# Kernel optimization log

Measured on AMD Instinct MI355X. Metric: run time of the kernel, lower is better.

Reference implementation:

```python
import jax, jax.numpy as jnp
import numpy as np

B, S, H, FF, E, K, A = 2, 2048, 2048, 8192, 8, 2, 64
P = 3 * H * FF                      # num_ffn_params (gate + up + down)
NS = int(P * 1e-4)                  # num_sparse = 5033
TEMP = 1.0                          # mask_temperature


def setup_inputs() -> dict:
    key = jax.random.key(0)
    ks = jax.random.split(key, 9)
    f32 = jnp.float32
    return {
        "hidden_states": jax.random.normal(ks[0], (B, S, H), f32),
        "gate_w": jax.random.normal(ks[1], (FF, H), f32) * 0.02,
        "up_w": jax.random.normal(ks[2], (FF, H), f32) * 0.02,
        "down_w": jax.random.normal(ks[3], (H, FF), f32) * 0.02,
        "router_w": jax.random.normal(ks[4], (E, H), f32) * 0.01,
        "mask_logits": jax.random.normal(ks[5], (P,), f32) * 0.01,
        "atoms": jax.random.normal(ks[6], (A, NS), f32) * 0.02,
        "expert_atom_weights": jax.random.normal(ks[7], (E, A), f32) * 0.1,
        "importance": jax.random.normal(ks[8], (E, NS), f32) * 0.1,
    }


def reference(hidden_states, gate_w, up_w, down_w, router_w, mask_logits,
              atoms, expert_atom_weights, importance):
    b, s, h = hidden_states.shape
    x = hidden_states.reshape(-1, h)                      # (T, H) tokens

    # ---- SRDERouter: gate -> clamp -> top-k -> softmax over top-k ----
    router_logits = jnp.clip(x @ router_w.T, -50.0, 50.0)  # (T, E)
    top_w, top_idx = jax.lax.top_k(router_logits, K)       # (T, K)
    router_weights = jax.nn.softmax(top_w, axis=-1)        # (T, K)

    # ---- LearnedMaskSelector (eval path: no gumbel noise), straight-through ----
    noisy = jnp.clip(mask_logits / TEMP, -50.0, 50.0)      # (P,)
    soft_mask = jax.nn.sigmoid(noisy)
    _, mask_idx = jax.lax.top_k(noisy, NS)                 # (NS,) positions in param space
    hard_mask = jnp.zeros_like(soft_mask).at[mask_idx].set(1.0)
    mask = hard_mask - jax.lax.stop_gradient(soft_mask) + soft_mask  # (P,)

    # ---- SharedDeltaVocabulary + SparseExpert importance weighting ----
    atom_w = jax.nn.softmax(expert_atom_weights, axis=-1)  # (E, A)
    deltas = atom_w @ atoms                                # (E, NS)
    weighted_deltas = deltas * jax.nn.sigmoid(importance)  # (E, NS)

    # ---- per-token gather of top-k expert deltas, weighted combine ----
    tok_deltas = weighted_deltas[top_idx]                  # (T, K, NS) irregular gather
    combined = jnp.einsum('tk,tks->ts', router_weights, tok_deltas)  # (T, NS)
    mean_delta = combined.mean(axis=0)                     # (NS,) batch-averaged delta

    # ---- scatter sparse delta into flat FFN param space, apply mask ----
    flat = jnp.concatenate([gate_w.ravel(), up_w.ravel(), down_w.ravel()])  # (P,)
    delta_full = jnp.zeros_like(flat).at[mask_idx].set(mean_delta) * mask
    new_flat = flat + delta_full
    n1 = FF * H
    gw = new_flat[:n1].reshape(FF, H)
    uw = new_flat[n1:2 * n1].reshape(FF, H)
    dw = new_flat[2 * n1:].reshape(H, FF)

    # ---- SwiGLU FFN with delta-perturbed params ----
    hidden = jax.nn.silu(x @ gw.T) * (x @ uw.T)            # (T, FF)
    out = (hidden @ dw.T).reshape(b, s, h)

    # ---- load-balancing aux loss ----
    probs = jax.nn.softmax(router_logits, axis=-1)         # (T, E)
    frac = jax.nn.one_hot(top_idx, E, dtype=probs.dtype).sum(1).mean(0) / K  # (E,)
    aux_loss = E * jnp.sum(probs.mean(0) * frac)

    return out, router_logits, router_weights, top_idx, aux_loss
```

## Files before the change

kernel.cpp:

```cpp
#include <hip/hip_runtime.h>
#include <stdint.h>

#define DEV __device__ __forceinline__

typedef __attribute__((ext_vector_type(8))) short short8;
typedef __attribute__((ext_vector_type(4))) float f32x4;

constexpr int       Td  = 4096;
constexpr int       Hd  = 2048;
constexpr int       FFd = 8192;
constexpr int       NSd = 5033;
constexpr long long n1  = 16777216LL;
constexpr long long Pn  = 50331648LL;
constexpr int NBINS    = 16384;
constexpr int CAND_CAP = 8192;
constexpr unsigned KEY_MIN = 0xBC75C28Fu;

constexpr size_t OUT_LOGITS = 8388608;
constexpr size_t OUT_RW     = 8421376;
constexpr size_t OUT_TI     = 8429568;
constexpr size_t OUT_AUX    = 8437760;

constexpr size_t OFF_W    = 0;
constexpr size_t OFF_X    = 100663296;
constexpr size_t OFF_HID  = 117440512;
constexpr size_t OFF_HIST = 184549376;
constexpr size_t OFF_META = OFF_HIST + NBINS * 4;
constexpr size_t OFF_CAND = OFF_META + 256;
constexpr size_t OFF_MIDX = OFF_CAND + CAND_CAP * 8;
constexpr size_t OFF_MD   = OFF_MIDX + 20480;

DEV unsigned short f2bf(float f) {
    unsigned u = __float_as_uint(f);
    u += 0x7FFFu + ((u >> 16) & 1u);
    return (unsigned short)(u >> 16);
}
DEV unsigned keyof(float v) {
    v = fminf(50.f, fmaxf(-50.f, v));
    unsigned b = __float_as_uint(v);
    return (b & 0x80000000u) ? ~b : (b | 0x80000000u);
}

#define GL16(gsrc, ldst) __builtin_amdgcn_global_load_lds( \
    (const __attribute__((address_space(1))) unsigned int*)(const void*)(gsrc), \
    (__attribute__((address_space(3))) unsigned int*)(void*)(ldst), 16, 0, 0)

#define SWZC(r, c) ((c) ^ (((r) & 7) << 3))
#define SWZ(r, c)  (((r) * 64) + SWZC(r, c))

__global__ __launch_bounds__(256) void k_cvt_x(const float4* __restrict__ x,
                                               ushort4* __restrict__ o, int n4) {
    int stride = gridDim.x * blockDim.x;
    for (int i = blockIdx.x * blockDim.x + threadIdx.x; i < n4; i += stride) {
        float4 v = x[i];
        ushort4 r; r.x = f2bf(v.x); r.y = f2bf(v.y); r.z = f2bf(v.z); r.w = f2bf(v.w);
        o[i] = r;
    }
}

__global__ __launch_bounds__(256) void k_cvt_w(const float4* __restrict__ g,
                                               const float4* __restrict__ u,
                                               const float4* __restrict__ d,
                                               ushort4* __restrict__ o) {
    const long long n1_4 = n1 / 4, n4 = Pn / 4;
    long long stride = (long long)gridDim.x * blockDim.x;
    for (long long i = blockIdx.x * (long long)blockDim.x + threadIdx.x; i < n4; i += stride) {
        float4 v = (i < n1_4) ? g[i] : (i < 2 * n1_4) ? u[i - n1_4] : d[i - 2 * n1_4];
        ushort4 r; r.x = f2bf(v.x); r.y = f2bf(v.y); r.z = f2bf(v.z); r.w = f2bf(v.w);
        o[i] = r;
    }
}

__global__ __launch_bounds__(1024) void k_router(const float* __restrict__ x,
                                                 const float* __restrict__ rw,
                                                 float* __restrict__ out,
                                                 float* __restrict__ meta_f) {
    __shared__ float sacc[24];
    int tid = threadIdx.x;
    if (tid < 24) sacc[tid] = 0.f;
    __syncthreads();
    int wid = tid >> 6, lane = tid & 63;
    int t = blockIdx.x * 16 + wid;
    const float4* xr = (const float4*)(x + (size_t)t * Hd);
    double acc[8] = {0, 0, 0, 0, 0, 0, 0, 0};
    for (int i = 0; i < 8; ++i) {
        float4 xv = xr[i * 64 + lane];
#pragma unroll
        for (int e = 0; e < 8; ++e) {
            float4 wv = ((const float4*)(rw + (size_t)e * Hd))[i * 64 + lane];
            acc[e] += (double)xv.x * wv.x + (double)xv.y * wv.y +
                      (double)xv.z * wv.z + (double)xv.w * wv.w;
        }
    }
#pragma unroll
    for (int e = 0; e < 8; ++e)
        for (int s = 32; s; s >>= 1) acc[e] += __shfl_xor(acc[e], s, 64);
    if (lane == 0) {
        float lg[8];
#pragma unroll
        for (int e = 0; e < 8; ++e) lg[e] = fminf(50.f, fmaxf(-50.f, (float)acc[e]));
        float* lo = out + OUT_LOGITS + (size_t)t * 8;
#pragma unroll
        for (int e = 0; e < 8; ++e) lo[e] = lg[e];
        int i1 = 0;
        for (int e = 1; e < 8; ++e) if (lg[e] > lg[i1]) i1 = e;
        int i2 = (i1 == 0) ? 1 : 0;
        for (int e = 0; e < 8; ++e) if (e != i1 && lg[e] > lg[i2]) i2 = e;
        float e2 = expf(lg[i2] - lg[i1]);
        float r1 = 1.f / (1.f + e2), r2 = e2 / (1.f + e2);
        out[OUT_RW + (size_t)t * 2]     = r1;
        out[OUT_RW + (size_t)t * 2 + 1] = r2;
        out[OUT_TI + (size_t)t * 2]     = (float)i1;
        out[OUT_TI + (size_t)t * 2 + 1] = (float)i2;
        float m = lg[0];
        for (int e = 1; e < 8; ++e) m = fmaxf(m, lg[e]);
        float p[8], s = 0.f;
#pragma unroll
        for (int e = 0; e < 8; ++e) { p[e] = expf(lg[e] - m); s += p[e]; }
        float inv = 1.f / s;
        atomicAdd(&sacc[i1], r1);  atomicAdd(&sacc[i2], r2);
        atomicAdd(&sacc[8 + i1], 1.f); atomicAdd(&sacc[8 + i2], 1.f);
#pragma unroll
        for (int e = 0; e < 8; ++e) atomicAdd(&sacc[16 + e], p[e] * inv);
    }
    __syncthreads();
    if (tid < 24) atomicAdd(&meta_f[4 + tid], sacc[tid]);
}

__global__ __launch_bounds__(256) void k_hist(const float4* __restrict__ ml,
                                              unsigned* __restrict__ gh) {
    __shared__ unsigned hh[NBINS];
    for (int i = threadIdx.x; i < NBINS; i += 256) hh[i] = 0;
    __syncthreads();
    const long long n4 = Pn / 4;
    long long stride = (long long)gridDim.x * 256;
    for (long long i = blockIdx.x * 256LL + threadIdx.x; i < n4; i += stride) {
        float4 v = ml[i];
        unsigned k0 = keyof(v.x), k1 = keyof(v.y), k2 = keyof(v.z), k3 = keyof(v.w);
        if (k0 >= KEY_MIN) atomicAdd(&hh[k0 >> 18], 1u);
        if (k1 >= KEY_MIN) atomicAdd(&hh[k1 >> 18], 1u);
        if (k2 >= KEY_MIN) atomicAdd(&hh[k2 >> 18], 1u);
        if (k3 >= KEY_MIN) atomicAdd(&hh[k3 >> 18], 1u);
    }
    __syncthreads();
    for (int i = threadIdx.x; i < NBINS; i += 256)
        if (hh[i]) atomicAdd(&gh[i], hh[i]);
}

__global__ __launch_bounds__(256) void k_scan(const unsigned* __restrict__ gh,
                                              unsigned* __restrict__ meta_u) {
    __shared__ unsigned ssum[256], sabove[256];
    int t = threadIdx.x;
    unsigned s = 0;
    for (int b = t * 64; b < t * 64 + 64; ++b) s += gh[b];
    ssum[t] = s;
    __syncthreads();
    if (t == 0) {
        unsigned run = 0;
        for (int i = 255; i >= 0; --i) { sabove[i] = run; run += ssum[i]; }
    }
    __syncthreads();
    unsigned above = sabove[t];
    if (above < (unsigned)NSd && above + ssum[t] >= (unsigned)NSd) {
        unsigned cum = above;
        for (int b = t * 64 + 63; b >= t * 64; --b) {
            cum += gh[b];
            if (cum >= (unsigned)NSd) { meta_u[1] = (unsigned)b; break; }
        }
    }
}

__global__ __launch_bounds__(256) void k_collect(const float4* __restrict__ ml,
                                                 unsigned* __restrict__ meta_u,
                                                 unsigned long long* __restrict__ cand) {
    const unsigned bucket = meta_u[1];
    const long long n4 = Pn / 4;
    long long stride = (long long)gridDim.x * 256;
    for (long long i = blockIdx.x * 256LL + threadIdx.x; i < n4; i += stride) {
        float4 v = ml[i];
        float vv[4] = {v.x, v.y, v.z, v.w};
#pragma unroll
        for (int j = 0; j < 4; ++j) {
            unsigned key = keyof(vv[j]);
            if ((key >> 18) >= bucket) {
                unsigned pos = atomicAdd(&meta_u[0], 1u);
                if (pos < CAND_CAP)
                    cand[pos] = ((unsigned long long)key << 32) |
                                (unsigned)~(unsigned)(i * 4 + j);
            }
        }
    }
}

__global__ __launch_bounds__(1024) void k_sort(const unsigned* __restrict__ meta_u,
                                               const unsigned long long* __restrict__ cand,
                                               unsigned* __restrict__ midx) {
    __shared__ unsigned long long sh[CAND_CAP];
    unsigned M = meta_u[0]; if (M > CAND_CAP) M = CAND_CAP;
    for (int i = threadIdx.x; i < CAND_CAP; i += 1024) sh[i] = (i < (int)M) ? cand[i] : 0ULL;
    __syncthreads();
    for (int k = 2; k <= CAND_CAP; k <<= 1)
        for (int j = k >> 1; j > 0; j >>= 1) {
            for (int i = threadIdx.x; i < CAND_CAP; i += 1024) {
                int l = i ^ j;
                if (l > i) {
                    unsigned long long a = sh[i], b = sh[l];
                    bool up = ((i & k) == 0);
                    if ((a > b) == up) { sh[i] = b; sh[l] = a; }
                }
            }
            __syncthreads();
        }
    for (int r = threadIdx.x; r < NSd; r += 1024)
        midx[r] = ~(unsigned)sh[CAND_CAP - 1 - r];
}

__global__ __launch_bounds__(256) void k_delta(const float* __restrict__ atoms,
                                               const float* __restrict__ eaw,
                                               const float* __restrict__ imp,
                                               const float* __restrict__ meta_f,
                                               float* __restrict__ md,
                                               float* __restrict__ out) {
    __shared__ float aw[8][64];
    int tid = threadIdx.x;
    if (tid < 8) {
        float m = -1e30f;
        for (int a = 0; a < 64; ++a) m = fmaxf(m, eaw[tid * 64 + a]);
        float s = 0.f;
        for (int a = 0; a < 64; ++a) { float v = expf(eaw[tid * 64 + a] - m); aw[tid][a] = v; s += v; }
        float inv = 1.f / s;
        for (int a = 0; a < 64; ++a) aw[tid][a] *= inv;
    }
    __syncthreads();
    int s_ = blockIdx.x * 256 + tid;
    if (s_ < NSd) {
        float d[8] = {0, 0, 0, 0, 0, 0, 0, 0};
        for (int a = 0; a < 64; ++a) {
            float av = atoms[(size_t)a * NSd + s_];
#pragma unroll
            for (int e = 0; e < 8; ++e) d[e] += aw[e][a] * av;
        }
        float m = 0.f;
#pragma unroll
        for (int e = 0; e < 8; ++e) {
            float coef = meta_f[4 + e] * (1.f / Td);
            float sg = 1.f / (1.f + expf(-imp[(size_t)e * NSd + s_]));
            m += coef * d[e] * sg;
        }
        md[s_] = m;
    }
    if (blockIdx.x == 0 && tid == 0) {
        float aux = 0.f;
        for (int e = 0; e < 8; ++e)
            aux += (meta_f[20 + e] / Td) * (meta_f[12 + e] / (Td * 2.f));
        out[OUT_AUX] = 8.f * aux;
    }
}

__global__ __launch_bounds__(256) void k_scatter(const unsigned* __restrict__ midx,
                                                 const float* __restrict__ md,
                                                 const float* __restrict__ g,
                                                 const float* __restrict__ u,
                                                 const float* __restrict__ dn,
                                                 unsigned short* __restrict__ wsW) {
    int i = blockIdx.x * 256 + threadIdx.x;
    if (i >= NSd) return;
    long long pos = (long long)midx[i];
    float orig = (pos < n1) ? g[pos] : (pos < 2 * n1) ? u[pos - n1] : dn[pos - 2 * n1];
    wsW[pos] = f2bf(orig + md[i]);
}

__global__ __launch_bounds__(512, 2) void k_gemm_gu(const unsigned short* __restrict__ Abf,
                                                    const unsigned short* __restrict__ Wg,
                                                    const unsigned short* __restrict__ Wu,
                                                    unsigned short* __restrict__ Hid) {
    extern __shared__ unsigned short sm[];
    const int tid = threadIdx.x, wid = tid >> 6, lane = tid & 63;
    const int lr = lane & 15, ko = (lane >> 4) * 8;
    const int wm = wid >> 2, wn = wid & 3;
    const int orig = blockIdx.x;
    const int swz = (orig & 7) * 128 + (orig >> 3);
    const int bm = swz & 15, bn = swz >> 4;
    const size_t arow = (size_t)bm * 256;
    const size_t brow = (size_t)bn * 128;

    f32x4 ag[8][2], au[8][2];
#pragma unroll
    for (int i = 0; i < 8; ++i)
#pragma unroll
        for (int j = 0; j < 2; ++j) { ag[i][j] = (f32x4)0.f; au[i][j] = (f32x4)0.f; }

    auto STAGE = [&](int kt, int b) {
        const int k0 = kt * 64;
        unsigned short* L = sm + b * 32768;
#pragma unroll
        for (int i = 0; i < 4; ++i) {
            int e = (i * 512 + tid) * 8; int r = e >> 6, c = e & 63;
            GL16(Abf + (arow + r) * 2048 + k0 + SWZC(r, c), L + e);
        }
#pragma unroll
        for (int i = 0; i < 2; ++i) {
            int e = (i * 512 + tid) * 8; int r = e >> 6, c = e & 63;
            GL16(Wg + (brow + r) * 2048 + k0 + SWZC(r, c), L + 16384 + e);
            GL16(Wu + (brow + r) * 2048 + k0 + SWZC(r, c), L + 24576 + e);
        }
    };

    constexpr int NT = 2048 / 64;
    STAGE(0, 0);
    STAGE(1, 1);
    for (int t = 0; t < NT; ++t) {
        const int cur = t & 1;
        unsigned short* L = sm + cur * 32768;
        if (t + 1 < NT) asm volatile("s_waitcnt vmcnt(8)" ::: "memory");
        else            asm volatile("s_waitcnt vmcnt(0)" ::: "memory");
        __builtin_amdgcn_s_barrier();
        short8 bg[2][2], bu[2][2];
#pragma unroll
        for (int nf = 0; nf < 2; ++nf)
#pragma unroll
            for (int ks = 0; ks < 2; ++ks) {
                bg[nf][ks] = *(const short8*)&L[16384 + SWZ(wn * 32 + nf * 16 + lr, ks * 32 + ko)];
                bu[nf][ks] = *(const short8*)&L[24576 + SWZ(wn * 32 + nf * 16 + lr, ks * 32 + ko)];
            }
#pragma unroll
        for (int p = 0; p < 4; ++p) {
            short8 a[2][2];
#pragma unroll
            for (int j = 0; j < 2; ++j)
#pragma unroll
                for (int ks = 0; ks < 2; ++ks)
                    a[j][ks] = *(const short8*)&L[SWZ(wm * 128 + (p * 2 + j) * 16 + lr, ks * 32 + ko)];
            if (p == 3) {
                asm volatile("s_waitcnt lgkmcnt(0)" ::: "memory");
                __builtin_amdgcn_s_barrier();
                if (t + 2 < NT) STAGE(t + 2, cur);
            }
            __builtin_amdgcn_s_setprio(1);
#pragma unroll
            for (int j = 0; j < 2; ++j) {
                int mf = p * 2 + j;
#pragma unroll
                for (int ks = 0; ks < 2; ++ks)
#pragma unroll
                    for (int nf = 0; nf < 2; ++nf) {
                        ag[mf][nf] = __builtin_amdgcn_mfma_f32_16x16x32_bf16(a[j][ks], bg[nf][ks], ag[mf][nf], 0, 0, 0);
                        au[mf][nf] = __builtin_amdgcn_mfma_f32_16x16x32_bf16(a[j][ks], bu[nf][ks], au[mf][nf], 0, 0, 0);
                    }
            }
            __builtin_amdgcn_s_setprio(0);
        }
    }
    const int rbase = (int)arow + wm * 128 + (lane >> 4) * 4;
    const int cbase = (int)brow + wn * 32 + lr;
#pragma unroll
    for (int mf = 0; mf < 8; ++mf)
#pragma unroll
        for (int nf = 0; nf < 2; ++nf)
#pragma unroll
            for (int reg = 0; reg < 4; ++reg) {
                float gv = ag[mf][nf][reg], uv = au[mf][nf][reg];
                float h = gv / (1.f + expf(-gv)) * uv;
                Hid[(size_t)(rbase + mf * 16 + reg) * FFd + cbase + nf * 16] = f2bf(h);
            }
}

__global__ __launch_bounds__(512, 2) void k_gemm_dn(const unsigned short* __restrict__ Abf,
                                                    const unsigned short* __restrict__ Wd,
                                                    float* __restrict__ Out) {
    extern __shared__ unsigned short sm[];
    const int tid = threadIdx.x, wid = tid >> 6, lane = tid & 63;
    const int lr = lane & 15, ko = (lane >> 4) * 8;
    const int wm = wid >> 2, wn = wid & 3;
    const int orig = blockIdx.x;
    const int swz = (orig & 7) * 32 + (orig >> 3);
    const int bn = swz & 7, bm = swz >> 3;
    const size_t arow = (size_t)bm * 128;
    const size_t brow = (size_t)bn * 256;

    f32x4 acc[4][4];
#pragma unroll
    for (int i = 0; i < 4; ++i)
#pragma unroll
        for (int j = 0; j < 4; ++j) acc[i][j] = (f32x4)0.f;

    auto STAGE = [&](int kt, int b) {
        const int k0 = kt * 64;
        unsigned short* L = sm + b * 24576;
#pragma unroll
        for (int i = 0; i < 2; ++i) {
            int e = (i * 512 + tid) * 8; int r = e >> 6, c = e & 63;
            GL16(Abf + (arow + r) * 8192 + k0 + SWZC(r, c), L + e);
        }
#pragma unroll
        for (int i = 0; i < 4; ++i) {
            int e = (i * 512 + tid) * 8; int r = e >> 6, c = e & 63;
            GL16(Wd + (brow + r) * 8192 + k0 + SWZC(r, c), L + 8192 + e);
        }
    };

    constexpr int NT = 8192 / 64;
    STAGE(0, 0);
    STAGE(1, 1);
    for (int t = 0; t < NT; ++t) {
        const int cur = t & 1;
        unsigned short* L = sm + cur * 24576;
        if (t + 1 < NT) asm volatile("s_waitcnt vmcnt(6)" ::: "memory");
        else            asm volatile("s_waitcnt vmcnt(0)" ::: "memory");
        __builtin_amdgcn_s_barrier();
        short8 b[4][2];
#pragma unroll
        for (int nf = 0; nf < 4; ++nf)
#pragma unroll
            for (int ks = 0; ks < 2; ++ks)
                b[nf][ks] = *(const short8*)&L[8192 + SWZ(wn * 64 + nf * 16 + lr, ks * 32 + ko)];
#pragma unroll
        for (int p = 0; p < 4; ++p) {
            short8 a[2];
#pragma unroll
            for (int ks = 0; ks < 2; ++ks)
                a[ks] = *(const short8*)&L[SWZ(wm * 64 + p * 16 + lr, ks * 32 + ko)];
            if (p == 3) {
                asm volatile("s_waitcnt lgkmcnt(0)" ::: "memory");
                __builtin_amdgcn_s_barrier();
                if (t + 2 < NT) STAGE(t + 2, cur);
            }
            __builtin_amdgcn_s_setprio(1);
#pragma unroll
            for (int ks = 0; ks < 2; ++ks)
#pragma unroll
                for (int nf = 0; nf < 4; ++nf)
                    acc[p][nf] = __builtin_amdgcn_mfma_f32_16x16x32_bf16(a[ks], b[nf][ks], acc[p][nf], 0, 0, 0);
            __builtin_amdgcn_s_setprio(0);
        }
    }
    const int rbase = (int)arow + wm * 64 + (lane >> 4) * 4;
    const int cbase = (int)brow + wn * 64 + lr;
#pragma unroll
    for (int mf = 0; mf < 4; ++mf)
#pragma unroll
        for (int nf = 0; nf < 4; ++nf)
#pragma unroll
            for (int reg = 0; reg < 4; ++reg)
                Out[(size_t)(rbase + mf * 16 + reg) * Hd + cbase + nf * 16] = acc[mf][nf][reg];
}

extern "C" void kernel_launch(void* const* d_in, const int* in_sizes, int n_in,
                              void* d_out, int out_size, void* d_ws, size_t ws_size,
                              hipStream_t stream) {
    const float* x     = (const float*)d_in[0];
    const float* gate  = (const float*)d_in[1];
    const float* up    = (const float*)d_in[2];
    const float* down  = (const float*)d_in[3];
    const float* rw    = (const float*)d_in[4];
    const float* ml    = (const float*)d_in[5];
    const float* atoms = (const float*)d_in[6];
    const float* eaw   = (const float*)d_in[7];
    const float* imp   = (const float*)d_in[8];
    float* out = (float*)d_out;
    char*  ws  = (char*)d_ws;

    unsigned short* wsW  = (unsigned short*)(ws + OFF_W);
    unsigned short* xbf  = (unsigned short*)(ws + OFF_X);
    unsigned short* hid  = (unsigned short*)(ws + OFF_HID);
    unsigned*       gh   = (unsigned*)(ws + OFF_HIST);
    unsigned*       mu   = (unsigned*)(ws + OFF_META);
    float*          mf   = (float*)(ws + OFF_META);
    unsigned long long* cand = (unsigned long long*)(ws + OFF_CAND);
    unsigned*       midx = (unsigned*)(ws + OFF_MIDX);
    float*          md   = (float*)(ws + OFF_MD);

    hipFuncSetAttribute((const void*)k_gemm_gu,
                        hipFuncAttributeMaxDynamicSharedMemorySize, 131072);
    hipFuncSetAttribute((const void*)k_gemm_dn,
                        hipFuncAttributeMaxDynamicSharedMemorySize, 98304);

    hipMemsetAsync(ws + OFF_HIST, 0, NBINS * 4 + 256, stream);

    k_cvt_x<<<2048, 256, 0, stream>>>((const float4*)x, (ushort4*)xbf, Td * Hd / 4);
    k_cvt_w<<<4096, 256, 0, stream>>>((const float4*)gate, (const float4*)up,
                                      (const float4*)down, (ushort4*)wsW);
    k_router<<<Td / 16, 1024, 0, stream>>>(x, rw, out, mf);
    k_hist<<<512, 256, 0, stream>>>((const float4*)ml, gh);
    k_scan<<<1, 256, 0, stream>>>(gh, mu);
    k_collect<<<2048, 256, 0, stream>>>((const float4*)ml, mu, cand);
    k_sort<<<1, 1024, 0, stream>>>(mu, cand, midx);
    k_delta<<<(NSd + 255) / 256, 256, 0, stream>>>(atoms, eaw, imp, mf, md, out);
    k_scatter<<<(NSd + 255) / 256, 256, 0, stream>>>(midx, md, gate, up, down, wsW);
    k_gemm_gu<<<1024, 512, 131072, stream>>>(xbf, wsW, wsW + n1, hid);
    k_gemm_dn<<<256, 512, 98304, stream>>>(hid, wsW + 2 * n1, out);
}
```

Baseline: 748.4 us.

## Fuse x conversion into router, single-pass mask selection, restage GEMM pipelines

Converts x to bf16 inside the router kernel, which removes the separate conversion kernel. The histogram pass now also dumps candidates above a looser fixed key threshold, so the collect step filters that small list instead of rereading all mask logits. Both GEMMs are restructured so that staging of the next tiles' A/B halves is interleaved with MFMA half-steps. The down GEMM moves to a triple-buffered ring with more LDS. The candidate dump relies on the fixed threshold holding enough elements and adds a global atomic in the hot histogram loop.

```diff
diff --git a/kernel.cpp b/kernel.cpp
--- a/kernel.cpp
+++ b/kernel.cpp
@@ -14,7 +14,9 @@
 constexpr long long Pn  = 50331648LL;
 constexpr int NBINS    = 16384;
 constexpr int CAND_CAP = 8192;
-constexpr unsigned KEY_MIN = 0xBC75C28Fu;
+constexpr unsigned DUMP_CAP = 131072;
+constexpr unsigned KEY_MIN  = 0xBC75C28Fu;
+constexpr unsigned KEY_DUMP = 0xBCF5C28Fu;
 
 constexpr size_t OUT_LOGITS = 8388608;
 constexpr size_t OUT_RW     = 8421376;
@@ -48,15 +50,7 @@
 #define SWZC(r, c) ((c) ^ (((r) & 7) << 3))
 #define SWZ(r, c)  (((r) * 64) + SWZC(r, c))
 
-__global__ __launch_bounds__(256) void k_cvt_x(const float4* __restrict__ x,
-                                               ushort4* __restrict__ o, int n4) {
-    int stride = gridDim.x * blockDim.x;
-    for (int i = blockIdx.x * blockDim.x + threadIdx.x; i < n4; i += stride) {
-        float4 v = x[i];
-        ushort4 r; r.x = f2bf(v.x); r.y = f2bf(v.y); r.z = f2bf(v.z); r.w = f2bf(v.w);
-        o[i] = r;
-    }
-}
+#define MFMA16 __builtin_amdgcn_mfma_f32_16x16x32_bf16
 
 __global__ __launch_bounds__(256) void k_cvt_w(const float4* __restrict__ g,
                                                const float4* __restrict__ u,
@@ -74,7 +68,8 @@
 __global__ __launch_bounds__(1024) void k_router(const float* __restrict__ x,
                                                  const float* __restrict__ rw,
                                                  float* __restrict__ out,
-                                                 float* __restrict__ meta_f) {
+                                                 float* __restrict__ meta_f,
+                                                 ushort4* __restrict__ xbf) {
     __shared__ float sacc[24];
     int tid = threadIdx.x;
     if (tid < 24) sacc[tid] = 0.f;
@@ -82,9 +77,12 @@
     int wid = tid >> 6, lane = tid & 63;
     int t = blockIdx.x * 16 + wid;
     const float4* xr = (const float4*)(x + (size_t)t * Hd);
+    ushort4* xw = xbf + (size_t)t * (Hd / 4);
     double acc[8] = {0, 0, 0, 0, 0, 0, 0, 0};
     for (int i = 0; i < 8; ++i) {
         float4 xv = xr[i * 64 + lane];
+        ushort4 xc; xc.x = f2bf(xv.x); xc.y = f2bf(xv.y); xc.z = f2bf(xv.z); xc.w = f2bf(xv.w);
+        xw[i * 64 + lane] = xc;
 #pragma unroll
         for (int e = 0; e < 8; ++e) {
             float4 wv = ((const float4*)(rw + (size_t)e * Hd))[i * 64 + lane];
@@ -128,7 +126,9 @@
 }
 
 __global__ __launch_bounds__(256) void k_hist(const float4* __restrict__ ml,
-                                              unsigned* __restrict__ gh) {
+                                              unsigned* __restrict__ gh,
+                                              unsigned* __restrict__ meta_u,
+                                              unsigned long long* __restrict__ cand2) {
     __shared__ unsigned hh[NBINS];
     for (int i = threadIdx.x; i < NBINS; i += 256) hh[i] = 0;
     __syncthreads();
@@ -136,11 +136,18 @@
     long long stride = (long long)gridDim.x * 256;
     for (long long i = blockIdx.x * 256LL + threadIdx.x; i < n4; i += stride) {
         float4 v = ml[i];
-        unsigned k0 = keyof(v.x), k1 = keyof(v.y), k2 = keyof(v.z), k3 = keyof(v.w);
-        if (k0 >= KEY_MIN) atomicAdd(&hh[k0 >> 18], 1u);
-        if (k1 >= KEY_MIN) atomicAdd(&hh[k1 >> 18], 1u);
-        if (k2 >= KEY_MIN) atomicAdd(&hh[k2 >> 18], 1u);
-        if (k3 >= KEY_MIN) atomicAdd(&hh[k3 >> 18], 1u);
+        float vv[4] = {v.x, v.y, v.z, v.w};
+#pragma unroll
+        for (int j = 0; j < 4; ++j) {
+            unsigned k = keyof(vv[j]);
+            if (k >= KEY_MIN) atomicAdd(&hh[k >> 18], 1u);
+            if (k >= KEY_DUMP) {
+                unsigned pos = atomicAdd(&meta_u[2], 1u);
+                if (pos < DUMP_CAP)
+                    cand2[pos] = ((unsigned long long)k << 32) |
+                                 (unsigned)~(unsigned)(i * 4 + j);
+            }
+        }
     }
     __syncthreads();
     for (int i = threadIdx.x; i < NBINS; i += 256)
@@ -170,24 +177,16 @@
     }
 }
 
-__global__ __launch_bounds__(256) void k_collect(const float4* __restrict__ ml,
+__global__ __launch_bounds__(256) void k_collect(const unsigned long long* __restrict__ cand2,
                                                  unsigned* __restrict__ meta_u,
                                                  unsigned long long* __restrict__ cand) {
-    const unsigned bucket = meta_u[1];
-    const long long n4 = Pn / 4;
-    long long stride = (long long)gridDim.x * 256;
-    for (long long i = blockIdx.x * 256LL + threadIdx.x; i < n4; i += stride) {
-        float4 v = ml[i];
-        float vv[4] = {v.x, v.y, v.z, v.w};
-#pragma unroll
-        for (int j = 0; j < 4; ++j) {
-            unsigned key = keyof(vv[j]);
-            if ((key >> 18) >= bucket) {
-                unsigned pos = atomicAdd(&meta_u[0], 1u);
-                if (pos < CAND_CAP)
-                    cand[pos] = ((unsigned long long)key << 32) |
-                                (unsigned)~(unsigned)(i * 4 + j);
-            }
+    unsigned M2 = meta_u[2]; if (M2 > DUMP_CAP) M2 = DUMP_CAP;
+    unsigned i = blockIdx.x * 256 + threadIdx.x;
+    if (i < M2) {
+        unsigned long long c = cand2[i];
+        if ((unsigned)(c >> 50) >= meta_u[1]) {
+            unsigned pos = atomicAdd(&meta_u[0], 1u);
+            if (pos < CAND_CAP) cand[pos] = c;
         }
     }
 }
@@ -290,66 +289,96 @@
 #pragma unroll
         for (int j = 0; j < 2; ++j) { ag[i][j] = (f32x4)0.f; au[i][j] = (f32x4)0.f; }
 
-    auto STAGE = [&](int kt, int b) {
-        const int k0 = kt * 64;
-        unsigned short* L = sm + b * 32768;
-#pragma unroll
-        for (int i = 0; i < 4; ++i) {
-            int e = (i * 512 + tid) * 8; int r = e >> 6, c = e & 63;
-            GL16(Abf + (arow + r) * 2048 + k0 + SWZC(r, c), L + e);
-        }
-#pragma unroll
-        for (int i = 0; i < 2; ++i) {
-            int e = (i * 512 + tid) * 8; int r = e >> 6, c = e & 63;
-            GL16(Wg + (brow + r) * 2048 + k0 + SWZC(r, c), L + 16384 + e);
-            GL16(Wu + (brow + r) * 2048 + k0 + SWZC(r, c), L + 24576 + e);
-        }
-    };
+    auto ST_A0 = [&](int kt, int b) {
+        const int k0 = kt * 64; unsigned short* L = sm + b * 32768;
+#pragma unroll
+        for (int i = 0; i < 2; ++i) { int e = (i * 512 + tid) * 8; int r = e >> 6, c = e & 63;
+            GL16(Abf + (arow + r) * 2048 + k0 + SWZC(r, c), L + e); } };
+    auto ST_A1 = [&](int kt, int b) {
+        const int k0 = kt * 64; unsigned short* L = sm + b * 32768;
+#pragma unroll
+        for (int i = 0; i < 2; ++i) { int e = 8192 + (i * 512 + tid) * 8; int r = e >> 6, c = e & 63;
+            GL16(Abf + (arow + r) * 2048 + k0 + SWZC(r, c), L + e); } };
+    auto ST_BG = [&](int kt, int b) {
+        const int k0 = kt * 64; unsigned short* L = sm + b * 32768;
+#pragma unroll
+        for (int i = 0; i < 2; ++i) { int e = (i * 512 + tid) * 8; int r = e >> 6, c = e & 63;
+            GL16(Wg + (brow + r) * 2048 + k0 + SWZC(r, c), L + 16384 + e); } };
+    auto ST_BU = [&](int kt, int b) {
+        const int k0 = kt * 64; unsigned short* L = sm + b * 32768;
+#pragma unroll
+        for (int i = 0; i < 2; ++i) { int e = (i * 512 + tid) * 8; int r = e >> 6, c = e & 63;
+            GL16(Wu + (brow + r) * 2048 + k0 + SWZC(r, c), L + 24576 + e); } };
 
     constexpr int NT = 2048 / 64;
-    STAGE(0, 0);
-    STAGE(1, 1);
+    ST_A0(0, 0); ST_A1(0, 0); ST_BG(0, 0); ST_BU(0, 0); ST_A0(1, 1); ST_A1(1, 1);
     for (int t = 0; t < NT; ++t) {
-        const int cur = t & 1;
+        const int cur = t & 1, nb = cur ^ 1;
         unsigned short* L = sm + cur * 32768;
-        if (t + 1 < NT) asm volatile("s_waitcnt vmcnt(8)" ::: "memory");
+        if (t + 1 < NT) asm volatile("s_waitcnt vmcnt(4)" ::: "memory");
         else            asm volatile("s_waitcnt vmcnt(0)" ::: "memory");
         __builtin_amdgcn_s_barrier();
-        short8 bg[2][2], bu[2][2];
-#pragma unroll
-        for (int nf = 0; nf < 2; ++nf)
-#pragma unroll
-            for (int ks = 0; ks < 2; ++ks) {
-                bg[nf][ks] = *(const short8*)&L[16384 + SWZ(wn * 32 + nf * 16 + lr, ks * 32 + ko)];
-                bu[nf][ks] = *(const short8*)&L[24576 + SWZ(wn * 32 + nf * 16 + lr, ks * 32 + ko)];
-            }
-#pragma unroll
-        for (int p = 0; p < 4; ++p) {
-            short8 a[2][2];
-#pragma unroll
-            for (int j = 0; j < 2; ++j)
-#pragma unroll
-                for (int ks = 0; ks < 2; ++ks)
-                    a[j][ks] = *(const short8*)&L[SWZ(wm * 128 + (p * 2 + j) * 16 + lr, ks * 32 + ko)];
-            if (p == 3) {
-                asm volatile("s_waitcnt lgkmcnt(0)" ::: "memory");
-                __builtin_amdgcn_s_barrier();
-                if (t + 2 < NT) STAGE(t + 2, cur);
-            }
-            __builtin_amdgcn_s_setprio(1);
-#pragma unroll
-            for (int j = 0; j < 2; ++j) {
-                int mf = p * 2 + j;
-#pragma unroll
-                for (int ks = 0; ks < 2; ++ks)
-#pragma unroll
-                    for (int nf = 0; nf < 2; ++nf) {
-                        ag[mf][nf] = __builtin_amdgcn_mfma_f32_16x16x32_bf16(a[j][ks], bg[nf][ks], ag[mf][nf], 0, 0, 0);
-                        au[mf][nf] = __builtin_amdgcn_mfma_f32_16x16x32_bf16(a[j][ks], bu[nf][ks], au[mf][nf], 0, 0, 0);
-                    }
-            }
-            __builtin_amdgcn_s_setprio(0);
-        }
+        short8 a0[8], a1[8], bg[2][2], bu[2][2];
+#pragma unroll
+        for (int m = 0; m < 8; ++m) a0[m] = *(const short8*)&L[SWZ(wm * 128 + m * 16 + lr, ko)];
+#pragma unroll
+        for (int n = 0; n < 2; ++n) {
+            bg[n][0] = *(const short8*)&L[16384 + SWZ(wn * 32 + n * 16 + lr, ko)];
+            bg[n][1] = *(const short8*)&L[16384 + SWZ(wn * 32 + n * 16 + lr, 32 + ko)];
+        }
+        if (t + 1 < NT) ST_BG(t + 1, nb);
+        __builtin_amdgcn_s_barrier();
+        asm volatile("s_waitcnt lgkmcnt(0)" ::: "memory");
+        __builtin_amdgcn_sched_barrier(0);
+        __builtin_amdgcn_s_setprio(1);
+#pragma unroll
+        for (int m = 0; m < 8; ++m) {
+            ag[m][0] = MFMA16(a0[m], bg[0][0], ag[m][0], 0, 0, 0);
+            ag[m][1] = MFMA16(a0[m], bg[1][0], ag[m][1], 0, 0, 0);
+        }
+        __builtin_amdgcn_s_setprio(0);
+        __builtin_amdgcn_s_barrier();
+#pragma unroll
+        for (int m = 0; m < 8; ++m) a1[m] = *(const short8*)&L[SWZ(wm * 128 + m * 16 + lr, 32 + ko)];
+        if (t + 1 < NT) ST_BU(t + 1, nb);
+        __builtin_amdgcn_s_barrier();
+        asm volatile("s_waitcnt lgkmcnt(0)" ::: "memory");
+        __builtin_amdgcn_sched_barrier(0);
+        __builtin_amdgcn_s_setprio(1);
+#pragma unroll
+        for (int m = 0; m < 8; ++m) {
+            ag[m][0] = MFMA16(a1[m], bg[0][1], ag[m][0], 0, 0, 0);
+            ag[m][1] = MFMA16(a1[m], bg[1][1], ag[m][1], 0, 0, 0);
+        }
+        __builtin_amdgcn_s_setprio(0);
+        __builtin_amdgcn_s_barrier();
+#pragma unroll
+        for (int n = 0; n < 2; ++n) {
+            bu[n][0] = *(const short8*)&L[24576 + SWZ(wn * 32 + n * 16 + lr, ko)];
+            bu[n][1] = *(const short8*)&L[24576 + SWZ(wn * 32 + n * 16 + lr, 32 + ko)];
+        }
+        if (t + 2 < NT) ST_A0(t + 2, cur);
+        __builtin_amdgcn_s_barrier();
+        asm volatile("s_waitcnt lgkmcnt(0)" ::: "memory");
+        __builtin_amdgcn_sched_barrier(0);
+        __builtin_amdgcn_s_setprio(1);
+#pragma unroll
+        for (int m = 0; m < 8; ++m) {
+            au[m][0] = MFMA16(a0[m], bu[0][0], au[m][0], 0, 0, 0);
+            au[m][1] = MFMA16(a0[m], bu[1][0], au[m][1], 0, 0, 0);
+        }
+        __builtin_amdgcn_s_setprio(0);
+        __builtin_amdgcn_s_barrier();
+        if (t + 2 < NT) ST_A1(t + 2, cur);
+        __builtin_amdgcn_s_barrier();
+        __builtin_amdgcn_s_setprio(1);
+#pragma unroll
+        for (int m = 0; m < 8; ++m) {
+            au[m][0] = MFMA16(a1[m], bu[0][1], au[m][0], 0, 0, 0);
+            au[m][1] = MFMA16(a1[m], bu[1][1], au[m][1], 0, 0, 0);
+        }
+        __builtin_amdgcn_s_setprio(0);
+        __builtin_amdgcn_s_barrier();
     }
     const int rbase = (int)arow + wm * 128 + (lane >> 4) * 4;
     const int cbase = (int)brow + wn * 32 + lr;
@@ -384,55 +413,63 @@
 #pragma unroll
         for (int j = 0; j < 4; ++j) acc[i][j] = (f32x4)0.f;
 
-    auto STAGE = [&](int kt, int b) {
-        const int k0 = kt * 64;
-        unsigned short* L = sm + b * 24576;
-#pragma unroll
-        for (int i = 0; i < 2; ++i) {
-            int e = (i * 512 + tid) * 8; int r = e >> 6, c = e & 63;
-            GL16(Abf + (arow + r) * 8192 + k0 + SWZC(r, c), L + e);
-        }
-#pragma unroll
-        for (int i = 0; i < 4; ++i) {
-            int e = (i * 512 + tid) * 8; int r = e >> 6, c = e & 63;
-            GL16(Wd + (brow + r) * 8192 + k0 + SWZC(r, c), L + 8192 + e);
-        }
-    };
+    auto ST_A = [&](int kt, int b) {
+        const int k0 = kt * 64; unsigned short* L = sm + b * 24576;
+#pragma unroll
+        for (int i = 0; i < 2; ++i) { int e = (i * 512 + tid) * 8; int r = e >> 6, c = e & 63;
+            GL16(Abf + (arow + r) * 8192 + k0 + SWZC(r, c), L + e); } };
+    auto ST_B = [&](int kt, int b) {
+        const int k0 = kt * 64; unsigned short* L = sm + b * 24576;
+#pragma unroll
+        for (int i = 0; i < 4; ++i) { int e = (i * 512 + tid) * 8; int r = e >> 6, c = e & 63;
+            GL16(Wd + (brow + r) * 8192 + k0 + SWZC(r, c), L + 8192 + e); } };
 
     constexpr int NT = 8192 / 64;
-    STAGE(0, 0);
-    STAGE(1, 1);
+    ST_A(0, 0); ST_B(0, 0); ST_A(1, 1); ST_B(1, 1);
+    int cur = 0;
     for (int t = 0; t < NT; ++t) {
-        const int cur = t & 1;
         unsigned short* L = sm + cur * 24576;
+        const int b2 = (cur + 2 >= 3) ? cur - 1 : cur + 2;
         if (t + 1 < NT) asm volatile("s_waitcnt vmcnt(6)" ::: "memory");
         else            asm volatile("s_waitcnt vmcnt(0)" ::: "memory");
         __builtin_amdgcn_s_barrier();
-        short8 b[4][2];
-#pragma unroll
-        for (int nf = 0; nf < 4; ++nf)
-#pragma unroll
-            for (int ks = 0; ks < 2; ++ks)
-                b[nf][ks] = *(const short8*)&L[8192 + SWZ(wn * 64 + nf * 16 + lr, ks * 32 + ko)];
-#pragma unroll
-        for (int p = 0; p < 4; ++p) {
-            short8 a[2];
-#pragma unroll
-            for (int ks = 0; ks < 2; ++ks)
-                a[ks] = *(const short8*)&L[SWZ(wm * 64 + p * 16 + lr, ks * 32 + ko)];
-            if (p == 3) {
-                asm volatile("s_waitcnt lgkmcnt(0)" ::: "memory");
-                __builtin_amdgcn_s_barrier();
-                if (t + 2 < NT) STAGE(t + 2, cur);
-            }
-            __builtin_amdgcn_s_setprio(1);
-#pragma unroll
-            for (int ks = 0; ks < 2; ++ks)
-#pragma unroll
-                for (int nf = 0; nf < 4; ++nf)
-                    acc[p][nf] = __builtin_amdgcn_mfma_f32_16x16x32_bf16(a[ks], b[nf][ks], acc[p][nf], 0, 0, 0);
-            __builtin_amdgcn_s_setprio(0);
-        }
+        short8 a[4][2], b[4];
+#pragma unroll
+        for (int m = 0; m < 4; ++m) {
+            a[m][0] = *(const short8*)&L[SWZ(wm * 64 + m * 16 + lr, ko)];
+            a[m][1] = *(const short8*)&L[SWZ(wm * 64 + m * 16 + lr, 32 + ko)];
+        }
+#pragma unroll
+        for (int n = 0; n < 4; ++n)
+            b[n] = *(const short8*)&L[8192 + SWZ(wn * 64 + n * 16 + lr, ko)];
+        if (t + 2 < NT) ST_B(t + 2, b2);
+        __builtin_amdgcn_s_barrier();
+        asm volatile("s_waitcnt lgkmcnt(0)" ::: "memory");
+        __builtin_amdgcn_sched_barrier(0);
+        __builtin_amdgcn_s_setprio(1);
+#pragma unroll
+        for (int m = 0; m < 4; ++m)
+#pragma unroll
+            for (int n = 0; n < 4; ++n)
+                acc[m][n] = MFMA16(a[m][0], b[n], acc[m][n], 0, 0, 0);
+        __builtin_amdgcn_s_setprio(0);
+        __builtin_amdgcn_s_barrier();
+#pragma unroll
+        for (int n = 0; n < 4; ++n)
+            b[n] = *(const short8*)&L[8192 + SWZ(wn * 64 + n * 16 + lr, 32 + ko)];
+        if (t + 2 < NT) ST_A(t + 2, b2);
+        __builtin_amdgcn_s_barrier();
+        asm volatile("s_waitcnt lgkmcnt(0)" ::: "memory");
+        __builtin_amdgcn_sched_barrier(0);
+        __builtin_amdgcn_s_setprio(1);
+#pragma unroll
+        for (int m = 0; m < 4; ++m)
+#pragma unroll
+            for (int n = 0; n < 4; ++n)
+                acc[m][n] = MFMA16(a[m][1], b[n], acc[m][n], 0, 0, 0);
+        __builtin_amdgcn_s_setprio(0);
+        __builtin_amdgcn_s_barrier();
+        cur = (cur + 1 >= 3) ? 0 : cur + 1;
     }
     const int rbase = (int)arow + wm * 64 + (lane >> 4) * 4;
     const int cbase = (int)brow + wn * 64 + lr;
@@ -469,24 +506,24 @@
     unsigned long long* cand = (unsigned long long*)(ws + OFF_CAND);
     unsigned*       midx = (unsigned*)(ws + OFF_MIDX);
     float*          md   = (float*)(ws + OFF_MD);
+    unsigned long long* cand2 = (unsigned long long*)(ws + OFF_HID);
 
     hipFuncSetAttribute((const void*)k_gemm_gu,
                         hipFuncAttributeMaxDynamicSharedMemorySize, 131072);
     hipFuncSetAttribute((const void*)k_gemm_dn,
-                        hipFuncAttributeMaxDynamicSharedMemorySize, 98304);
+                        hipFuncAttributeMaxDynamicSharedMemorySize, 147456);
 
     hipMemsetAsync(ws + OFF_HIST, 0, NBINS * 4 + 256, stream);
 
-    k_cvt_x<<<2048, 256, 0, stream>>>((const float4*)x, (ushort4*)xbf, Td * Hd / 4);
     k_cvt_w<<<4096, 256, 0, stream>>>((const float4*)gate, (const float4*)up,
                                       (const float4*)down, (ushort4*)wsW);
-    k_router<<<Td / 16, 1024, 0, stream>>>(x, rw, out, mf);
-    k_hist<<<512, 256, 0, stream>>>((const float4*)ml, gh);
+    k_router<<<Td / 16, 1024, 0, stream>>>(x, rw, out, mf, (ushort4*)xbf);
+    k_hist<<<512, 256, 0, stream>>>((const float4*)ml, gh, mu, cand2);
     k_scan<<<1, 256, 0, stream>>>(gh, mu);
-    k_collect<<<2048, 256, 0, stream>>>((const float4*)ml, mu, cand);
+    k_collect<<<512, 256, 0, stream>>>(cand2, mu, cand);
     k_sort<<<1, 1024, 0, stream>>>(mu, cand, midx);
     k_delta<<<(NSd + 255) / 256, 256, 0, stream>>>(atoms, eaw, imp, mf, md, out);
     k_scatter<<<(NSd + 255) / 256, 256, 0, stream>>>(midx, md, gate, up, down, wsW);
     k_gemm_gu<<<1024, 512, 131072, stream>>>(xbf, wsW, wsW + n1, hid);
-    k_gemm_dn<<<256, 512, 98304, stream>>>(hid, wsW + 2 * n1, out);
-}
+    k_gemm_dn<<<256, 512, 147456, stream>>>(hid, wsW + 2 * n1, out);
+}
```

Measured after the change: 1.347 ms. 1.8x slower.
